# Kernel tuning notes

Measured on AMD Instinct MI355X. Metric: run time of the kernel, lower is better.

Reference implementation:

```python
import jax, jax.numpy as jnp
import numpy as np

B, NE, NN, L = 64, 256, 1024, 512
F_IN, HID = 128, 128
VOCAB = 50000
ALPHA = 0.2
NEG = -9.0e15


def _leaky(z):
    return jnp.where(z >= 0, z, ALPHA * z)


def hga_layer(x, adj, W, W2, W3, a, a2, wc, transfer, concat):
    # x: [B, NN, Fin], adj: [B, NE, NN] (hyperedge incidence)
    O = W2.shape[1]
    x4 = x @ W2                      # [B, NN, O]
    if transfer:
        x = x @ W                    # [B, NN, O]
    # node->edge attention: score depends only on node k (query is shared word_context)
    s0 = wc[0] @ a[:O, 0]            # scalar
    e1 = _leaky(x4 @ a[O:, 0] + s0)  # [B, NN]
    e1 = jnp.broadcast_to(e1[:, None, :], adj.shape)          # [B, NE, NN]
    att_edge = jax.nn.softmax(jnp.where(adj > 0, e1, NEG), axis=2)
    edge = att_edge @ x              # [B, NE, O]
    edge4 = edge @ W3                # [B, NE, O]
    # edge->node attention: query = node feat x4[k], key = edge feat edge4[j]
    e2 = _leaky((x4 @ a2[:O, 0])[:, None, :] + (edge4 @ a2[O:, 0])[:, :, None])  # [B, NE, NN]
    att_node = jax.nn.softmax(jnp.where(adj > 0, e2, NEG).transpose(0, 2, 1), axis=2)  # [B, NN, NE]
    node = att_node @ edge           # [B, NN, O]
    return jax.nn.elu(node) if concat else node


def setup_inputs() -> dict:
    key = jax.random.key(0)
    ks = jax.random.split(key, 16)
    stdv = 1.0 / np.sqrt(HID)
    u = lambda k, shape: jax.random.uniform(k, shape, jnp.float32, -stdv, stdv)
    inp = {
        "items": jax.random.randint(ks[0], (B, NN), 0, VOCAB),
        "alias_inputs": jax.random.randint(ks[1], (B, L), 0, NN),
        "node_masks": jnp.ones((B, L), jnp.float32),
        "adj": jax.random.randint(ks[2], (B, NE, NN), 0, 2).astype(jnp.float32),
        "emb": jax.random.normal(ks[3], (VOCAB, F_IN), jnp.float32),
        # layer 1 (transfer=False, concat=True)
        "w2_1": u(ks[4], (F_IN, HID)),
        "w3_1": u(ks[5], (HID, HID)),
        "a_1": u(ks[6], (2 * HID, 1)),
        "a2_1": u(ks[7], (2 * HID, 1)),
        "wc_1": u(ks[8], (1, HID)),
        # layer 2 (transfer=True, concat=False)
        "w_2": u(ks[9], (HID, HID)),
        "w2_2": u(ks[10], (HID, HID)),
        "w3_2": u(ks[11], (HID, HID)),
        "a_2": u(ks[12], (2 * HID, 1)),
        "a2_2": u(ks[13], (2 * HID, 1)),
        "wc_2": u(ks[14], (1, HID)),
        "ln_g": jnp.ones((HID,), jnp.float32),
        "ln_b": jnp.zeros((HID,), jnp.float32),
    }
    return inp


def reference(items, alias_inputs, node_masks, adj, emb,
              w2_1, w3_1, a_1, a2_1, wc_1,
              w_2, w2_2, w3_2, a_2, a2_2, wc_2,
              ln_g, ln_b):
    hidden = emb[items]                                        # [B, NN, F]
    x = hga_layer(hidden, adj, None, w2_1, w3_1, a_1, a2_1, wc_1,
                  transfer=False, concat=True)
    x = hga_layer(x, adj, w_2, w2_2, w3_2, a_2, a2_2, wc_2,
                  transfer=True, concat=False)                 # [B, NN, HID]
    seq = jnp.take_along_axis(x, alias_inputs[:, :, None], axis=1)  # [B, L, HID]
    m = node_masks[:, :, None]
    h = seq * m
    b = jnp.sum(h * m, axis=-2) / jnp.sum(node_masks, -1, keepdims=True)  # [B, HID]
    mu = jnp.mean(b, -1, keepdims=True)
    var = jnp.mean((b - mu) ** 2, -1, keepdims=True)
    return (b - mu) / jnp.sqrt(var + 1e-6) * ln_g + ln_b
```

## Files before the change

kernel.cpp:

```cpp
#include <hip/hip_runtime.h>
#include <hip/hip_bf16.h>

typedef __hip_bfloat16 bf16;
typedef __attribute__((ext_vector_type(8))) unsigned short u16x8;
typedef __attribute__((ext_vector_type(4))) unsigned short u16x4;
typedef __attribute__((ext_vector_type(4))) float f32x4;
typedef __attribute__((ext_vector_type(8))) short bf16x8;

#define B_   64
#define NE_  256
#define NN_  1024
#define L_   512
#define HID_ 128
#define ALPHA_ 0.2f

__device__ __forceinline__ float bfu(unsigned short u){
  unsigned int x = ((unsigned int)u) << 16;
  union { unsigned int i; float f; } c; c.i = x; return c.f;
}
__device__ __forceinline__ unsigned short f2b(float f){
  bf16 h = __float2bfloat16(f);
  union { bf16 b; unsigned short u; } c; c.b = h; return c.u;
}
__device__ __forceinline__ int swz(int r, int c){ return (c ^ (r & 3) ^ ((r >> 2) & 3)) & 3; }

__global__ void k_consts(const float* w2_1, const float* w3_1,
                         const float* a_1, const float* a2_1, const float* wc_1,
                         const float* w2_2, const float* w3_2,
                         const float* a_2, const float* a2_2, const float* wc_2,
                         const float* w_2,
                         float* consts, unsigned short* W2T)
{
  int blk = blockIdx.x, t = threadIdx.x;
  __shared__ float red[128];
  if (blk < 6) {
    const float* M; const float* v;
    switch (blk) {
      case 0: M = w2_1; v = a_1  + 128; break;
      case 1: M = w2_1; v = a2_1;       break;
      case 2: M = w3_1; v = a2_1 + 128; break;
      case 3: M = w2_2; v = a_2  + 128; break;
      case 4: M = w2_2; v = a2_2;       break;
      default: M = w3_2; v = a2_2 + 128; break;
    }
    float acc = 0.f;
    for (int o = 0; o < 128; ++o) acc += M[t*128 + o] * v[o];
    consts[blk*128 + t] = acc;
  } else if (blk < 8) {
    const float* wc = (blk == 6) ? wc_1 : wc_2;
    const float* a  = (blk == 6) ? a_1  : a_2;
    red[t] = wc[t] * a[t];
    __syncthreads();
    for (int s = 64; s > 0; s >>= 1) { if (t < s) red[t] += red[t + s]; __syncthreads(); }
    if (t == 0) consts[768 + (blk - 6)] = red[0];
  } else {
    for (int k = 0; k < 128; ++k) W2T[t*128 + k] = f2b(w_2[k*128 + t]);
  }
}

__global__ void k_prep(const float* __restrict__ adj,
                       unsigned long long* __restrict__ ADJBb,
                       unsigned long long* __restrict__ ADJTb)
{
  __shared__ unsigned char tile[64][68];
  __shared__ unsigned short pa[64][4];
  __shared__ unsigned short pt[64][4];
  int b  = blockIdx.z;
  int e0 = blockIdx.y * 64;
  int n0 = blockIdx.x * 64;
  int t  = threadIdx.x;
  int lr = t >> 2, lc0 = (t & 3) * 16;
  const float* src = adj + ((long)b*NE_ + e0 + lr)*NN_ + n0 + lc0;
  unsigned int mA = 0;
  #pragma unroll
  for (int j = 0; j < 16; j += 4) {
    f32x4 v = *(const f32x4*)(src + j);
    #pragma unroll
    for (int k = 0; k < 4; ++k) {
      unsigned char u = (v[k] != 0.f) ? 1 : 0;
      tile[lr][lc0+j+k] = u;
      mA |= ((unsigned int)u) << (j+k);
    }
  }
  pa[lr][t & 3] = (unsigned short)mA;
  __syncthreads();
  unsigned int mT = 0;
  #pragma unroll
  for (int j = 0; j < 16; ++j) mT |= ((unsigned int)tile[lc0 + j][lr]) << j;
  pt[lr][t & 3] = (unsigned short)mT;
  __syncthreads();
  if (t < 64) {
    unsigned long long wA = (unsigned long long)pa[t][0]
                          | ((unsigned long long)pa[t][1] << 16)
                          | ((unsigned long long)pa[t][2] << 32)
                          | ((unsigned long long)pa[t][3] << 48);
    ADJBb[((long)b*NE_ + e0 + t)*(NN_/64) + (n0 >> 6)] = wA;
    unsigned long long wT = (unsigned long long)pt[t][0]
                          | ((unsigned long long)pt[t][1] << 16)
                          | ((unsigned long long)pt[t][2] << 32)
                          | ((unsigned long long)pt[t][3] << 48);
    ADJTb[((long)b*NN_ + n0 + t)*(NE_/64) + (e0 >> 6)] = wT;
  }
}

__global__ void k_fproj(const float* __restrict__ emb, const int* __restrict__ gitems,
                        const float* __restrict__ consts,
                        float* __restrict__ w1, float* __restrict__ f1,
                        unsigned short* __restrict__ YT)
{
  __shared__ float ce1s[128], cf1s[128];
  __shared__ __attribute__((aligned(16))) unsigned short T[64][132];
  int b = blockIdx.y, n0 = blockIdx.x * 64, t = threadIdx.x;
  if (t < 128) { ce1s[t] = consts[t]; cf1s[t] = consts[128 + t]; }
  __syncthreads();
  int r = t >> 2, h0 = (t & 3) * 32;
  long row = (long)b*NN_ + n0 + r;
  float s0 = consts[768];
  float xv[32];
  const float* sp = emb + (long)gitems[row]*HID_ + h0;
  #pragma unroll
  for (int j = 0; j < 32; j += 4) {
    f32x4 v = *(const f32x4*)(sp + j);
    #pragma unroll
    for (int k = 0; k < 4; ++k) xv[j+k] = v[k];
  }
  float p1 = 0.f, p2 = 0.f;
  #pragma unroll
  for (int j = 0; j < 32; ++j) { p1 += xv[j]*ce1s[h0+j]; p2 += xv[j]*cf1s[h0+j]; }
  p1 += __shfl_xor(p1, 1, 4); p1 += __shfl_xor(p1, 2, 4);
  p2 += __shfl_xor(p2, 1, 4); p2 += __shfl_xor(p2, 2, 4);
  float z = p1 + s0; z = (z >= 0.f) ? z : ALPHA_*z;
  float w = __expf(z);
  if ((t & 3) == 0) { w1[row] = w; f1[row] = p2; }
  #pragma unroll
  for (int j = 0; j < 32; j += 4) {
    u16x4 o;
    #pragma unroll
    for (int k = 0; k < 4; ++k) o[k] = f2b(w * xv[j+k]);
    *(u16x4*)&T[r][h0+j] = o;
  }
  __syncthreads();
  int h = t >> 1, nh = (t & 1) * 32;
  unsigned short* dst = YT + ((long)b*HID_ + h)*NN_ + n0 + nh;
  #pragma unroll
  for (int j = 0; j < 32; j += 8) {
    u16x8 o;
    #pragma unroll
    for (int k = 0; k < 8; ++k) o[k] = T[nh+j+k][h];
    *(u16x8*)&dst[j] = o;
  }
}

template<int TRANSFER>
__global__ __launch_bounds__(256) void k_gemm_edge(
    const unsigned char* __restrict__ ADJ8,
    const unsigned short* __restrict__ YT,
    const float* __restrict__ w1v,
    const float* __restrict__ consts, int layer,
    const unsigned short* __restrict__ W2T,
    unsigned short* __restrict__ ET,
    float* __restrict__ f2o)
{
  __shared__ __attribute__((aligned(16))) unsigned short SM[12288];
  __shared__ float dsum[64];
  const int id = blockIdx.x;
  const int b = id & 63;
  const long e0 = (long)(id >> 6) * 64;
  const int t = threadIdx.x;
  const int lane = t & 63;
  const int w = t >> 6, wm = w >> 1, wn = w & 1;
  const int r4 = t >> 2, c4 = t & 3;
  const int lr = lane & 15, g = lane >> 4;

  f32x4 acc[2][4];
  #pragma unroll
  for (int i = 0; i < 2; ++i)
    #pragma unroll
    for (int j = 0; j < 4; ++j) acc[i][j] = (f32x4){0.f,0.f,0.f,0.f};

  const unsigned char*  Ab = ADJ8 + ((long)b*NE_ + e0 + r4)*(NN_ >> 3);
  const unsigned short* Bb = YT + (long)b*HID_*NN_;
  const float*          wb = w1v + (long)b*NN_;

  unsigned int ab; u16x8 bv0, bv1; f32x4 wv0, wv1;
  float dot = 0.f;

  auto stage = [&](int kc) {
    ab  = Ab[(kc >> 3) + c4];
    wv0 = *(const f32x4*)(wb + kc + c4*8);
    wv1 = *(const f32x4*)(wb + kc + c4*8 + 4);
    bv0 = *(const u16x8*)(Bb + (long)r4*NN_ + kc + c4*8);
    bv1 = *(const u16x8*)(Bb + (long)(64+r4)*NN_ + kc + c4*8);
  };
  auto commit = [&](int buf) {
    u16x8 av;
    #pragma unroll
    for (int j = 0; j < 8; ++j) {
      unsigned int bit = (ab >> j) & 1u;
      av[j] = bit ? (unsigned short)0x3F80 : (unsigned short)0;
      float wj = (j < 4) ? wv0[j] : wv1[j-4];
      dot += bit ? wj : 0.f;
    }
    *(u16x8*)&SM[buf*2048 + r4*32 + swz(r4,c4)*8] = av;
    *(u16x8*)&SM[4096 + buf*4096 + r4*32 + swz(r4,c4)*8] = bv0;
    *(u16x8*)&SM[4096 + buf*4096 + (64+r4)*32 + swz(64+r4,c4)*8] = bv1;
  };

  stage(0); commit(0);
  int cur = 0;
  const int NIT = NN_/32;
  for (int it = 0; it < NIT; ++it) {
    __syncthreads();
    if (it+1 < NIT) stage((it+1)*32);
    const unsigned short* AsB = &SM[cur*2048];
    const unsigned short* BsB = &SM[4096 + cur*4096];
    bf16x8 af[2], bfr[4];
    #pragma unroll
    for (int mt = 0; mt < 2; ++mt) {
      int r = wm*32 + mt*16 + lr;
      af[mt] = *(const bf16x8*)&AsB[r*32 + swz(r,g)*8];
    }
    #pragma unroll
    for (int nt = 0; nt < 4; ++nt) {
      int n = wn*64 + nt*16 + lr;
      bfr[nt] = *(const bf16x8*)&BsB[n*32 + swz(n,g)*8];
    }
    #pragma unroll
    for (int mt = 0; mt < 2; ++mt)
      #pragma unroll
      for (int nt = 0; nt < 4; ++nt)
        acc[mt][nt] = __builtin_amdgcn_mfma_f32_16x16x32_bf16(af[mt], bfr[nt], acc[mt][nt], 0, 0, 0);
    if (it+1 < NIT) { commit(cur^1); cur ^= 1; }
  }
  dot += __shfl_down(dot, 2, 4); dot += __shfl_down(dot, 1, 4);
  if ((lane & 3) == 0) dsum[r4] = dot;
  __syncthreads();
  #pragma unroll
  for (int mt = 0; mt < 2; ++mt)
    #pragma unroll
    for (int nt = 0; nt < 4; ++nt) {
      int col = wn*64 + nt*16 + lr;
      #pragma unroll
      for (int q = 0; q < 4; ++q) {
        int rl = wm*32 + mt*16 + g*4 + q;
        SM[rl*136 + col] = f2b(acc[mt][nt][q] / dsum[rl]);
      }
    }
  __syncthreads();
  if (TRANSFER) {
    f32x4 acc2[2][4];
    #pragma unroll
    for (int i = 0; i < 2; ++i)
      #pragma unroll
      for (int j = 0; j < 4; ++j) acc2[i][j] = (f32x4){0.f,0.f,0.f,0.f};
    #pragma unroll
    for (int kc2 = 0; kc2 < 4; ++kc2) {
      bf16x8 af[2], bfr[4];
      #pragma unroll
      for (int mt = 0; mt < 2; ++mt) {
        int r = wm*32 + mt*16 + lr;
        af[mt] = *(const bf16x8*)&SM[r*136 + kc2*32 + g*8];
      }
      #pragma unroll
      for (int nt = 0; nt < 4; ++nt) {
        int n = wn*64 + nt*16 + lr;
        bfr[nt] = *(const bf16x8*)(W2T + n*128 + kc2*32 + g*8);
      }
      #pragma unroll
      for (int mt = 0; mt < 2; ++mt)
        #pragma unroll
        for (int nt = 0; nt < 4; ++nt)
          acc2[mt][nt] = __builtin_amdgcn_mfma_f32_16x16x32_bf16(af[mt], bfr[nt], acc2[mt][nt], 0, 0, 0);
    }
    __syncthreads();
    #pragma unroll
    for (int mt = 0; mt < 2; ++mt)
      #pragma unroll
      for (int nt = 0; nt < 4; ++nt) {
        int col = wn*64 + nt*16 + lr;
        #pragma unroll
        for (int q = 0; q < 4; ++q) {
          int rl = wm*32 + mt*16 + g*4 + q;
          SM[rl*136 + col] = f2b(acc2[mt][nt][q]);
        }
      }
    __syncthreads();
  }
  {
    const float* cf2 = consts + layer*384 + 256;
    int r = t >> 2, h0 = (t & 3) * 32;
    float p = 0.f;
    #pragma unroll
    for (int j = 0; j < 32; ++j) p += bfu(SM[r*136 + h0 + j]) * cf2[h0 + j];
    p += __shfl_down(p, 2, 4); p += __shfl_down(p, 1, 4);
    if ((t & 3) == 0) f2o[(long)b*NE_ + e0 + r] = p;
  }
  {
    int h = t >> 1, eh = (t & 1) * 32;
    unsigned short* dst = ET + ((long)b*HID_ + h)*NE_ + e0 + eh;
    #pragma unroll
    for (int j = 0; j < 32; j += 8) {
      u16x8 o;
      #pragma unroll
      for (int k = 0; k < 8; ++k) o[k] = SM[(eh+j+k)*136 + h];
      *(u16x8*)&dst[j] = o;
    }
  }
}

template<int EPI>
__global__ __launch_bounds__(256, 2) void k_gemm_att(
    const unsigned char* __restrict__ ADJ8,
    const unsigned short* __restrict__ ET,
    const float* __restrict__ f1v, const float* __restrict__ f2v,
    const float* __restrict__ consts,
    unsigned short* __restrict__ YTout, float* __restrict__ w1o, float* __restrict__ f1o,
    const float* __restrict__ wcount, float* __restrict__ pooled)
{
  __shared__ __attribute__((aligned(16))) unsigned short SM[12288];
  __shared__ float dsum[64];
  __shared__ float colsum[128];
  __shared__ float wrow[64];
  const int id = blockIdx.x;
  const int b = id & 63;
  const long m0 = (long)(id >> 6) * 64;
  const int t = threadIdx.x;
  const int lane = t & 63;
  const int w = t >> 6, wm = w >> 1, wn = w & 1;
  const int r4 = t >> 2, c4 = t & 3;
  const int lr = lane & 15, g = lane >> 4;

  f32x4 acc[2][4];
  #pragma unroll
  for (int i = 0; i < 2; ++i)
    #pragma unroll
    for (int j = 0; j < 4; ++j) acc[i][j] = (f32x4){0.f,0.f,0.f,0.f};

  const float f1r = f1v[(long)b*NN_ + m0 + r4];
  const unsigned char*  Ab = ADJ8 + ((long)b*NN_ + m0 + r4)*(NE_ >> 3);
  const unsigned short* Bb = ET + (long)b*HID_*NE_;
  const float* f2p = f2v + (long)b*NE_;

  unsigned int ab; u16x8 bv0, bv1; f32x4 fv0, fv1;
  float dot = 0.f;

  auto stage = [&](int kc) {
    ab  = Ab[(kc >> 3) + c4];
    fv0 = *(const f32x4*)(f2p + kc + c4*8);
    fv1 = *(const f32x4*)(f2p + kc + c4*8 + 4);
    bv0 = *(const u16x8*)(Bb + (long)r4*NE_ + kc + c4*8);
    bv1 = *(const u16x8*)(Bb + (long)(64+r4)*NE_ + kc + c4*8);
  };
  auto commit = [&](int buf) {
    u16x8 av;
    #pragma unroll
    for (int j = 0; j < 8; ++j) {
      unsigned int bit = (ab >> j) & 1u;
      float z = f1r + ((j < 4) ? fv0[j] : fv1[j-4]);
      z = (z >= 0.f) ? z : ALPHA_ * z;
      float wt = bit ? __expf(z) : 0.f;
      unsigned short us = f2b(wt);
      av[j] = us; dot += bfu(us);
    }
    *(u16x8*)&SM[buf*2048 + r4*32 + swz(r4,c4)*8] = av;
    *(u16x8*)&SM[4096 + buf*4096 + r4*32 + swz(r4,c4)*8] = bv0;
    *(u16x8*)&SM[4096 + buf*4096 + (64+r4)*32 + swz(64+r4,c4)*8] = bv1;
  };

  stage(0); commit(0);
  int cur = 0;
  const int NIT = NE_/32;
  for (int it = 0; it < NIT; ++it) {
    __syncthreads();
    if (it+1 < NIT) stage((it+1)*32);
    const unsigned short* AsB = &SM[cur*2048];
    const unsigned short* BsB = &SM[4096 + cur*4096];
    bf16x8 af[2], bfr[4];
    #pragma unroll
    for (int mt = 0; mt < 2; ++mt) {
      int r = wm*32 + mt*16 + lr;
      af[mt] = *(const bf16x8*)&AsB[r*32 + swz(r,g)*8];
    }
    #pragma unroll
    for (int nt = 0; nt < 4; ++nt) {
      int n = wn*64 + nt*16 + lr;
      bfr[nt] = *(const bf16x8*)&BsB[n*32 + swz(n,g)*8];
    }
    #pragma unroll
    for (int mt = 0; mt < 2; ++mt)
      #pragma unroll
      for (int nt = 0; nt < 4; ++nt)
        acc[mt][nt] = __builtin_amdgcn_mfma_f32_16x16x32_bf16(af[mt], bfr[nt], acc[mt][nt], 0, 0, 0);
    if (it+1 < NIT) { commit(cur^1); cur ^= 1; }
  }
  dot += __shfl_down(dot, 2, 4); dot += __shfl_down(dot, 1, 4);
  if ((lane & 3) == 0) dsum[r4] = dot;
  if (EPI == 2 && t < 128) colsum[t] = 0.f;
  __syncthreads();

  if (EPI == 1) {
    #pragma unroll
    for (int mt = 0; mt < 2; ++mt)
      #pragma unroll
      for (int nt = 0; nt < 4; ++nt) {
        int col = wn*64 + nt*16 + lr;
        #pragma unroll
        for (int q = 0; q < 4; ++q) {
          int rl = wm*32 + mt*16 + g*4 + q;
          float v = acc[mt][nt][q] / dsum[rl];
          v = (v > 0.f) ? v : expm1f(v);
          SM[rl*136 + col] = f2b(v);
        }
      }
    __syncthreads();
    {
      const float* ce1 = consts + 384;
      const float* cf1 = consts + 512;
      int r = t >> 2, h0 = (t & 3) * 32;
      float p1 = 0.f, p2 = 0.f;
      #pragma unroll
      for (int j = 0; j < 32; ++j) {
        float xv = bfu(SM[r*136 + h0 + j]);
        p1 += xv * ce1[h0 + j];
        p2 += xv * cf1[h0 + j];
      }
      p1 += __shfl_down(p1, 2, 4); p1 += __shfl_down(p1, 1, 4);
      p2 += __shfl_down(p2, 2, 4); p2 += __shfl_down(p2, 1, 4);
      if ((t & 3) == 0) {
        float z = p1 + consts[769];
        z = (z >= 0.f) ? z : ALPHA_ * z;
        float wv = __expf(z);
        wrow[r] = wv;
        w1o[(long)b*NN_ + m0 + r] = wv;
        f1o[(long)b*NN_ + m0 + r] = p2;
      }
    }
    __syncthreads();
    {
      int h = t >> 1, nh = (t & 1) * 32;
      unsigned short* dst = YTout + ((long)b*HID_ + h)*NN_ + m0 + nh;
      #pragma unroll
      for (int j = 0; j < 32; j += 8) {
        u16x8 o;
        #pragma unroll
        for (int k = 0; k < 8; ++k) {
          int rr = nh + j + k;
          o[k] = f2b(wrow[rr] * bfu(SM[rr*136 + h]));
        }
        *(u16x8*)&dst[j] = o;
      }
    }
  } else {
    float psum[4] = {0.f, 0.f, 0.f, 0.f};
    #pragma unroll
    for (int mt = 0; mt < 2; ++mt)
      #pragma unroll
      for (int q = 0; q < 4; ++q) {
        int rl = wm*32 + mt*16 + g*4 + q;
        float wc = wcount[(long)b*NN_ + m0 + rl];
        float inv = wc / dsum[rl];
        #pragma unroll
        for (int nt = 0; nt < 4; ++nt) psum[nt] += inv * acc[mt][nt][q];
      }
    #pragma unroll
    for (int nt = 0; nt < 4; ++nt) atomicAdd(&colsum[wn*64 + nt*16 + lr], psum[nt]);
    __syncthreads();
    if (t < 128) atomicAdd(&pooled[(long)b*HID_ + t], colsum[t]);
  }
}

__global__ void k_zero(float* __restrict__ p, int n)
{
  int i = blockIdx.x*256 + threadIdx.x;
  if (i < n) p[i] = 0.f;
}

__global__ void k_wcount(const int* __restrict__ alias, const float* __restrict__ masks,
                         float* __restrict__ wcount, float* __restrict__ msum)
{
  int b = blockIdx.x, t = threadIdx.x;
  float m = masks[b*L_ + t];
  int idx = alias[b*L_ + t];
  atomicAdd(&wcount[(long)b*NN_ + idx], m*m);
  float s = m;
  #pragma unroll
  for (int sh = 32; sh > 0; sh >>= 1) s += __shfl_down(s, sh);
  __shared__ float red[8];
  if ((t & 63) == 0) red[t >> 6] = s;
  __syncthreads();
  if (t == 0) { float tot = 0.f; for (int i = 0; i < 8; ++i) tot += red[i]; msum[b] = tot; }
}

__global__ void k_ln(const float* __restrict__ pooled, const float* __restrict__ msum,
                     const float* __restrict__ ln_g, const float* __restrict__ ln_b,
                     float* __restrict__ out)
{
  int b = blockIdx.x, t = threadIdx.x;
  __shared__ float sr[2];
  float bv = pooled[b*HID_ + t] / msum[b];
  int lane = t & 63;
  float p = bv;
  #pragma unroll
  for (int s = 32; s > 0; s >>= 1) p += __shfl_xor(p, s);
  if (lane == 0) sr[t >> 6] = p;
  __syncthreads();
  float mu = (sr[0] + sr[1]) * (1.f / HID_);
  float dv = bv - mu;
  p = dv * dv;
  #pragma unroll
  for (int s = 32; s > 0; s >>= 1) p += __shfl_xor(p, s);
  __syncthreads();
  if (lane == 0) sr[t >> 6] = p;
  __syncthreads();
  float var = (sr[0] + sr[1]) * (1.f / HID_);
  out[b*HID_ + t] = dv / sqrtf(var + 1e-6f) * ln_g[t] + ln_b[t];
}

extern "C" void kernel_launch(void* const* d_in, const int* in_sizes, int n_in,
                              void* d_out, int out_size, void* d_ws, size_t ws_size,
                              hipStream_t stream)
{
  const int*   items = (const int*)d_in[0];
  const int*   alias = (const int*)d_in[1];
  const float* masks = (const float*)d_in[2];
  const float* adj   = (const float*)d_in[3];
  const float* emb   = (const float*)d_in[4];
  const float* w2_1  = (const float*)d_in[5];
  const float* w3_1  = (const float*)d_in[6];
  const float* a_1   = (const float*)d_in[7];
  const float* a2_1  = (const float*)d_in[8];
  const float* wc_1  = (const float*)d_in[9];
  const float* w_2   = (const float*)d_in[10];
  const float* w2_2  = (const float*)d_in[11];
  const float* w3_2  = (const float*)d_in[12];
  const float* a_2   = (const float*)d_in[13];
  const float* a2_2  = (const float*)d_in[14];
  const float* wc_2  = (const float*)d_in[15];
  const float* ln_g  = (const float*)d_in[16];
  const float* ln_b  = (const float*)d_in[17];
  float* out = (float*)d_out;

  char* ws = (char*)d_ws;
  size_t off = 0;
  auto alloc = [&](size_t bytes) -> void* {
    void* p = ws + off; off += (bytes + 255) / 256 * 256; return p;
  };
  unsigned long long* ADJBb = (unsigned long long*)alloc((size_t)B_*NE_*(NN_/8));
  unsigned long long* ADJTb = (unsigned long long*)alloc((size_t)B_*NN_*(NE_/8));
  unsigned short* YT   = (unsigned short*)alloc((size_t)B_*HID_*NN_*2);
  unsigned short* ET   = (unsigned short*)alloc((size_t)B_*HID_*NE_*2);
  float* wcount= (float*)alloc((size_t)B_*NN_*4);
  float* pooled= (float*)alloc((size_t)B_*HID_*4);
  float* w1L1  = (float*)alloc((size_t)B_*NN_*4);
  float* f1L1  = (float*)alloc((size_t)B_*NN_*4);
  float* w1L2  = (float*)alloc((size_t)B_*NN_*4);
  float* f1L2  = (float*)alloc((size_t)B_*NN_*4);
  float* f2    = (float*)alloc((size_t)B_*NE_*4);
  float* msum  = (float*)alloc(B_*4);
  float* consts= (float*)alloc(772*4);
  unsigned short* W2T = (unsigned short*)alloc((size_t)HID_*HID_*2);
  if (off > ws_size) return;

  const int kZeroN = B_*NN_ + B_*HID_;

  k_consts<<<9, 128, 0, stream>>>(w2_1, w3_1, a_1, a2_1, wc_1, w2_2, w3_2, a_2, a2_2, wc_2,
                                  w_2, consts, W2T);
  k_zero<<<(kZeroN + 255)/256, 256, 0, stream>>>(wcount, kZeroN);
  k_wcount<<<B_, L_, 0, stream>>>(alias, masks, wcount, msum);
  k_prep<<<dim3(NN_/64, NE_/64, B_), 256, 0, stream>>>(adj, ADJBb, ADJTb);

  k_fproj<<<dim3(NN_/64, B_), 256, 0, stream>>>(emb, items, consts, w1L1, f1L1, YT);
  k_gemm_edge<0><<<B_*(NE_/64), 256, 0, stream>>>((const unsigned char*)ADJBb, YT, w1L1,
        consts, 0, W2T, ET, f2);
  k_gemm_att<1><<<B_*(NN_/64), 256, 0, stream>>>((const unsigned char*)ADJTb, ET, f1L1, f2,
        consts, YT, w1L2, f1L2, nullptr, nullptr);

  k_gemm_edge<1><<<B_*(NE_/64), 256, 0, stream>>>((const unsigned char*)ADJBb, YT, w1L2,
        consts, 1, W2T, ET, f2);
  k_gemm_att<2><<<B_*(NN_/64), 256, 0, stream>>>((const unsigned char*)ADJTb, ET, f1L2, f2,
        consts, nullptr, nullptr, nullptr, wcount, pooled);

  k_ln<<<B_, HID_, 0, stream>>>(pooled, msum, ln_g, ln_b, out);
}
```

Before: 133.6 us.

## Merge front-end prep kernels into one launch with block-range dispatch

```diff
diff --git a/kernel.cpp b/kernel.cpp
--- a/kernel.cpp
+++ b/kernel.cpp
@@ -24,130 +24,184 @@
 }
 __device__ __forceinline__ int swz(int r, int c){ return (c ^ (r & 3) ^ ((r >> 2) & 3)) & 3; }
 
-__global__ void k_consts(const float* w2_1, const float* w3_1,
-                         const float* a_1, const float* a2_1, const float* wc_1,
-                         const float* w2_2, const float* w3_2,
-                         const float* a_2, const float* a2_2, const float* wc_2,
-                         const float* w_2,
-                         float* consts, unsigned short* W2T)
+__global__ __launch_bounds__(256) void k_front(
+    const float* __restrict__ adj,
+    unsigned long long* __restrict__ ADJBb, unsigned long long* __restrict__ ADJTb,
+    const float* __restrict__ emb, const int* __restrict__ items,
+    const float* __restrict__ w2_1, const float* __restrict__ w3_1,
+    const float* __restrict__ a_1,  const float* __restrict__ a2_1,
+    const float* __restrict__ wc_1,
+    const float* __restrict__ w_2,
+    const float* __restrict__ w2_2, const float* __restrict__ w3_2,
+    const float* __restrict__ a_2,  const float* __restrict__ a2_2,
+    const float* __restrict__ wc_2,
+    const int* __restrict__ alias, const float* __restrict__ masks,
+    float* __restrict__ w1L1, float* __restrict__ f1L1,
+    unsigned short* __restrict__ YT,
+    float* __restrict__ consts, unsigned short* __restrict__ W2T,
+    float* __restrict__ wcount, float* __restrict__ msum, float* __restrict__ pooled)
 {
-  int blk = blockIdx.x, t = threadIdx.x;
-  __shared__ float red[128];
-  if (blk < 6) {
-    const float* M; const float* v;
-    switch (blk) {
-      case 0: M = w2_1; v = a_1  + 128; break;
-      case 1: M = w2_1; v = a2_1;       break;
-      case 2: M = w3_1; v = a2_1 + 128; break;
-      case 3: M = w2_2; v = a_2  + 128; break;
-      case 4: M = w2_2; v = a2_2;       break;
-      default: M = w3_2; v = a2_2 + 128; break;
-    }
-    float acc = 0.f;
-    for (int o = 0; o < 128; ++o) acc += M[t*128 + o] * v[o];
-    consts[blk*128 + t] = acc;
-  } else if (blk < 8) {
-    const float* wc = (blk == 6) ? wc_1 : wc_2;
-    const float* a  = (blk == 6) ? a_1  : a_2;
-    red[t] = wc[t] * a[t];
-    __syncthreads();
-    for (int s = 64; s > 0; s >>= 1) { if (t < s) red[t] += red[t + s]; __syncthreads(); }
-    if (t == 0) consts[768 + (blk - 6)] = red[0];
+  __shared__ __attribute__((aligned(16))) unsigned char SMEM[18432];
+  const int id = blockIdx.x;
+  const int t  = threadIdx.x;
+
+  if (id < 4096) {
+    unsigned char (*tile)[68] = (unsigned char(*)[68])SMEM;
+    unsigned short (*pa)[4] = (unsigned short(*)[4])(SMEM + 4608);
+    unsigned short (*pt)[4] = (unsigned short(*)[4])(SMEM + 5120);
+    int b  = id >> 6;
+    int e0 = ((id >> 4) & 3) * 64;
+    int n0 = (id & 15) * 64;
+    int lr = t >> 2, lc0 = (t & 3) * 16;
+    const float* src = adj + ((long)b*NE_ + e0 + lr)*NN_ + n0 + lc0;
+    unsigned int mA = 0;
+    #pragma unroll
+    for (int j = 0; j < 16; j += 4) {
+      f32x4 v = *(const f32x4*)(src + j);
+      #pragma unroll
+      for (int k = 0; k < 4; ++k) {
+        unsigned char u = (v[k] != 0.f) ? 1 : 0;
+        tile[lr][lc0+j+k] = u;
+        mA |= ((unsigned int)u) << (j+k);
+      }
+    }
+    pa[lr][t & 3] = (unsigned short)mA;
+    __syncthreads();
+    unsigned int mT = 0;
+    #pragma unroll
+    for (int j = 0; j < 16; ++j) mT |= ((unsigned int)tile[lc0 + j][lr]) << j;
+    pt[lr][t & 3] = (unsigned short)mT;
+    __syncthreads();
+    if (t < 64) {
+      unsigned long long wA = (unsigned long long)pa[t][0]
+                            | ((unsigned long long)pa[t][1] << 16)
+                            | ((unsigned long long)pa[t][2] << 32)
+                            | ((unsigned long long)pa[t][3] << 48);
+      ADJBb[((long)b*NE_ + e0 + t)*(NN_/64) + (n0 >> 6)] = wA;
+      unsigned long long wT = (unsigned long long)pt[t][0]
+                            | ((unsigned long long)pt[t][1] << 16)
+                            | ((unsigned long long)pt[t][2] << 32)
+                            | ((unsigned long long)pt[t][3] << 48);
+      ADJTb[((long)b*NN_ + n0 + t)*(NE_/64) + (e0 >> 6)] = wT;
+    }
+  } else if (id < 5120) {
+    float* ce1s = (float*)SMEM;
+    float* cf1s = (float*)(SMEM + 512);
+    float* s0s  = (float*)(SMEM + 1024);
+    unsigned short (*T)[132] = (unsigned short(*)[132])(SMEM + 1040 + 8);
+    T = (unsigned short(*)[132])(SMEM + 1056);
+    {
+      int rr = t & 127;
+      const float* Mrow = w2_1 + rr*128;
+      const float* vv = (t < 128) ? (a_1 + 128) : a2_1;
+      float acc = 0.f;
+      #pragma unroll 4
+      for (int o = 0; o < 128; o += 4) {
+        f32x4 m = *(const f32x4*)(Mrow + o);
+        f32x4 x = *(const f32x4*)(vv + o);
+        acc += m[0]*x[0] + m[1]*x[1] + m[2]*x[2] + m[3]*x[3];
+      }
+      if (t < 128) ce1s[rr] = acc; else cf1s[rr] = acc;
+      if (t < 64) {
+        float s = wc_1[t]*a_1[t] + wc_1[t+64]*a_1[t+64];
+        #pragma unroll
+        for (int sh = 32; sh > 0; sh >>= 1) s += __shfl_xor(s, sh);
+        if (t == 0) s0s[0] = s;
+      }
+    }
+    __syncthreads();
+    int fid = id - 4096;
+    int b = fid >> 4, n0 = (fid & 15) * 64;
+    int r = t >> 2, h0 = (t & 3) * 32;
+    long row = (long)b*NN_ + n0 + r;
+    float s0 = s0s[0];
+    float xv[32];
+    const float* sp = emb + (long)items[row]*HID_ + h0;
+    #pragma unroll
+    for (int j = 0; j < 32; j += 4) {
+      f32x4 v = *(const f32x4*)(sp + j);
+      #pragma unroll
+      for (int k = 0; k < 4; ++k) xv[j+k] = v[k];
+    }
+    float p1 = 0.f, p2 = 0.f;
+    #pragma unroll
+    for (int j = 0; j < 32; ++j) { p1 += xv[j]*ce1s[h0+j]; p2 += xv[j]*cf1s[h0+j]; }
+    p1 += __shfl_xor(p1, 1, 4); p1 += __shfl_xor(p1, 2, 4);
+    p2 += __shfl_xor(p2, 1, 4); p2 += __shfl_xor(p2, 2, 4);
+    float z = p1 + s0; z = (z >= 0.f) ? z : ALPHA_*z;
+    float w = __expf(z);
+    if ((t & 3) == 0) { w1L1[row] = w; f1L1[row] = p2; }
+    #pragma unroll
+    for (int j = 0; j < 32; j += 4) {
+      u16x4 o;
+      #pragma unroll
+      for (int k = 0; k < 4; ++k) o[k] = f2b(w * xv[j+k]);
+      *(u16x4*)&T[r][h0+j] = o;
+    }
+    __syncthreads();
+    int h = t >> 1, nh = (t & 1) * 32;
+    unsigned short* dst = YT + ((long)b*HID_ + h)*NN_ + n0 + nh;
+    #pragma unroll
+    for (int j = 0; j < 32; j += 8) {
+      u16x8 o;
+      #pragma unroll
+      for (int k = 0; k < 8; ++k) o[k] = T[nh+j+k][h];
+      *(u16x8*)&dst[j] = o;
+    }
+  } else if (id < 5129) {
+    float* red = (float*)SMEM;
+    int blk = id - 5120;
+    if (t >= 128) { __syncthreads(); return; }
+    if (blk < 6) {
+      const float* M; const float* v;
+      switch (blk) {
+        case 0: M = w2_1; v = a_1  + 128; break;
+        case 1: M = w2_1; v = a2_1;       break;
+        case 2: M = w3_1; v = a2_1 + 128; break;
+        case 3: M = w2_2; v = a_2  + 128; break;
+        case 4: M = w2_2; v = a2_2;       break;
+        default: M = w3_2; v = a2_2 + 128; break;
+      }
+      float acc = 0.f;
+      for (int o = 0; o < 128; ++o) acc += M[t*128 + o] * v[o];
+      consts[blk*128 + t] = acc;
+      __syncthreads();
+    } else if (blk < 8) {
+      const float* wc = (blk == 6) ? wc_1 : wc_2;
+      const float* a  = (blk == 6) ? a_1  : a_2;
+      red[t] = wc[t] * a[t];
+      __syncthreads();
+      for (int s = 64; s > 0; s >>= 1) { if (t < s) red[t] += red[t + s]; __syncthreads(); }
+      if (t == 0) consts[768 + (blk - 6)] = red[0];
+    } else {
+      for (int k = 0; k < 128; ++k) W2T[t*128 + k] = f2b(w_2[k*128 + t]);
+      __syncthreads();
+    }
+  } else if (id < 5193) {
+    float* wc = (float*)SMEM;
+    float* red = (float*)(SMEM + 4096);
+    int b = id - 5129;
+    #pragma unroll
+    for (int j = 0; j < 4; ++j) wc[t + j*256] = 0.f;
+    __syncthreads();
+    float s = 0.f;
+    #pragma unroll
+    for (int j = 0; j < 2; ++j) {
+      int l = t + j*256;
+      float m = masks[b*L_ + l];
+      int idx = alias[b*L_ + l];
+      atomicAdd(&wc[idx], m*m);
+      s += m;
+    }
+    #pragma unroll
+    for (int sh = 32; sh > 0; sh >>= 1) s += __shfl_xor(s, sh);
+    if ((t & 63) == 0) red[t >> 6] = s;
+    __syncthreads();
+    if (t == 0) msum[b] = red[0] + red[1] + red[2] + red[3];
+    #pragma unroll
+    for (int j = 0; j < 4; ++j) wcount[(long)b*NN_ + t + j*256] = wc[t + j*256];
   } else {
-    for (int k = 0; k < 128; ++k) W2T[t*128 + k] = f2b(w_2[k*128 + t]);
-  }
-}
-
-__global__ void k_prep(const float* __restrict__ adj,
-                       unsigned long long* __restrict__ ADJBb,
-                       unsigned long long* __restrict__ ADJTb)
-{
-  __shared__ unsigned char tile[64][68];
-  __shared__ unsigned short pa[64][4];
-  __shared__ unsigned short pt[64][4];
-  int b  = blockIdx.z;
-  int e0 = blockIdx.y * 64;
-  int n0 = blockIdx.x * 64;
-  int t  = threadIdx.x;
-  int lr = t >> 2, lc0 = (t & 3) * 16;
-  const float* src = adj + ((long)b*NE_ + e0 + lr)*NN_ + n0 + lc0;
-  unsigned int mA = 0;
-  #pragma unroll
-  for (int j = 0; j < 16; j += 4) {
-    f32x4 v = *(const f32x4*)(src + j);
-    #pragma unroll
-    for (int k = 0; k < 4; ++k) {
-      unsigned char u = (v[k] != 0.f) ? 1 : 0;
-      tile[lr][lc0+j+k] = u;
-      mA |= ((unsigned int)u) << (j+k);
-    }
-  }
-  pa[lr][t & 3] = (unsigned short)mA;
-  __syncthreads();
-  unsigned int mT = 0;
-  #pragma unroll
-  for (int j = 0; j < 16; ++j) mT |= ((unsigned int)tile[lc0 + j][lr]) << j;
-  pt[lr][t & 3] = (unsigned short)mT;
-  __syncthreads();
-  if (t < 64) {
-    unsigned long long wA = (unsigned long long)pa[t][0]
-                          | ((unsigned long long)pa[t][1] << 16)
-                          | ((unsigned long long)pa[t][2] << 32)
-                          | ((unsigned long long)pa[t][3] << 48);
-    ADJBb[((long)b*NE_ + e0 + t)*(NN_/64) + (n0 >> 6)] = wA;
-    unsigned long long wT = (unsigned long long)pt[t][0]
-                          | ((unsigned long long)pt[t][1] << 16)
-                          | ((unsigned long long)pt[t][2] << 32)
-                          | ((unsigned long long)pt[t][3] << 48);
-    ADJTb[((long)b*NN_ + n0 + t)*(NE_/64) + (e0 >> 6)] = wT;
-  }
-}
-
-__global__ void k_fproj(const float* __restrict__ emb, const int* __restrict__ gitems,
-                        const float* __restrict__ consts,
-                        float* __restrict__ w1, float* __restrict__ f1,
-                        unsigned short* __restrict__ YT)
-{
-  __shared__ float ce1s[128], cf1s[128];
-  __shared__ __attribute__((aligned(16))) unsigned short T[64][132];
-  int b = blockIdx.y, n0 = blockIdx.x * 64, t = threadIdx.x;
-  if (t < 128) { ce1s[t] = consts[t]; cf1s[t] = consts[128 + t]; }
-  __syncthreads();
-  int r = t >> 2, h0 = (t & 3) * 32;
-  long row = (long)b*NN_ + n0 + r;
-  float s0 = consts[768];
-  float xv[32];
-  const float* sp = emb + (long)gitems[row]*HID_ + h0;
-  #pragma unroll
-  for (int j = 0; j < 32; j += 4) {
-    f32x4 v = *(const f32x4*)(sp + j);
-    #pragma unroll
-    for (int k = 0; k < 4; ++k) xv[j+k] = v[k];
-  }
-  float p1 = 0.f, p2 = 0.f;
-  #pragma unroll
-  for (int j = 0; j < 32; ++j) { p1 += xv[j]*ce1s[h0+j]; p2 += xv[j]*cf1s[h0+j]; }
-  p1 += __shfl_xor(p1, 1, 4); p1 += __shfl_xor(p1, 2, 4);
-  p2 += __shfl_xor(p2, 1, 4); p2 += __shfl_xor(p2, 2, 4);
-  float z = p1 + s0; z = (z >= 0.f) ? z : ALPHA_*z;
-  float w = __expf(z);
-  if ((t & 3) == 0) { w1[row] = w; f1[row] = p2; }
-  #pragma unroll
-  for (int j = 0; j < 32; j += 4) {
-    u16x4 o;
-    #pragma unroll
-    for (int k = 0; k < 4; ++k) o[k] = f2b(w * xv[j+k]);
-    *(u16x4*)&T[r][h0+j] = o;
-  }
-  __syncthreads();
-  int h = t >> 1, nh = (t & 1) * 32;
-  unsigned short* dst = YT + ((long)b*HID_ + h)*NN_ + n0 + nh;
-  #pragma unroll
-  for (int j = 0; j < 32; j += 8) {
-    u16x8 o;
-    #pragma unroll
-    for (int k = 0; k < 8; ++k) o[k] = T[nh+j+k][h];
-    *(u16x8*)&dst[j] = o;
+    for (int i = t; i < B_*HID_; i += 256) pooled[i] = 0.f;
   }
 }
 
@@ -467,28 +521,6 @@
     __syncthreads();
     if (t < 128) atomicAdd(&pooled[(long)b*HID_ + t], colsum[t]);
   }
-}
-
-__global__ void k_zero(float* __restrict__ p, int n)
-{
-  int i = blockIdx.x*256 + threadIdx.x;
-  if (i < n) p[i] = 0.f;
-}
-
-__global__ void k_wcount(const int* __restrict__ alias, const float* __restrict__ masks,
-                         float* __restrict__ wcount, float* __restrict__ msum)
-{
-  int b = blockIdx.x, t = threadIdx.x;
-  float m = masks[b*L_ + t];
-  int idx = alias[b*L_ + t];
-  atomicAdd(&wcount[(long)b*NN_ + idx], m*m);
-  float s = m;
-  #pragma unroll
-  for (int sh = 32; sh > 0; sh >>= 1) s += __shfl_down(s, sh);
-  __shared__ float red[8];
-  if ((t & 63) == 0) red[t >> 6] = s;
-  __syncthreads();
-  if (t == 0) { float tot = 0.f; for (int i = 0; i < 8; ++i) tot += red[i]; msum[b] = tot; }
 }
 
 __global__ void k_ln(const float* __restrict__ pooled, const float* __restrict__ msum,
@@ -561,15 +593,10 @@
   unsigned short* W2T = (unsigned short*)alloc((size_t)HID_*HID_*2);
   if (off > ws_size) return;
 
-  const int kZeroN = B_*NN_ + B_*HID_;
-
-  k_consts<<<9, 128, 0, stream>>>(w2_1, w3_1, a_1, a2_1, wc_1, w2_2, w3_2, a_2, a2_2, wc_2,
-                                  w_2, consts, W2T);
-  k_zero<<<(kZeroN + 255)/256, 256, 0, stream>>>(wcount, kZeroN);
-  k_wcount<<<B_, L_, 0, stream>>>(alias, masks, wcount, msum);
-  k_prep<<<dim3(NN_/64, NE_/64, B_), 256, 0, stream>>>(adj, ADJBb, ADJTb);
-
-  k_fproj<<<dim3(NN_/64, B_), 256, 0, stream>>>(emb, items, consts, w1L1, f1L1, YT);
+  k_front<<<5194, 256, 0, stream>>>(adj, ADJBb, ADJTb, emb, items,
+        w2_1, w3_1, a_1, a2_1, wc_1, w_2, w2_2, w3_2, a_2, a2_2, wc_2,
+        alias, masks, w1L1, f1L1, YT, consts, W2T, wcount, msum, pooled);
+
   k_gemm_edge<0><<<B_*(NE_/64), 256, 0, stream>>>((const unsigned char*)ADJBb, YT, w1L1,
         consts, 0, W2T, ET, f2);
   k_gemm_att<1><<<B_*(NN_/64), 256, 0, stream>>>((const unsigned char*)ADJTb, ET, f1L1, f2,
```

New measurement: 139.5 us. 4.4% more time.

## Merge setup kernels into one launch and rewrite adjacency bit-packing transpose

Applied to the files above, without the earlier changes.

```diff
diff --git a/kernel.cpp b/kernel.cpp
--- a/kernel.cpp
+++ b/kernel.cpp
@@ -24,82 +24,112 @@
 }
 __device__ __forceinline__ int swz(int r, int c){ return (c ^ (r & 3) ^ ((r >> 2) & 3)) & 3; }
 
-__global__ void k_consts(const float* w2_1, const float* w3_1,
-                         const float* a_1, const float* a2_1, const float* wc_1,
-                         const float* w2_2, const float* w3_2,
-                         const float* a_2, const float* a2_2, const float* wc_2,
-                         const float* w_2,
-                         float* consts, unsigned short* W2T)
-{
+__global__ void k_small(const float* __restrict__ w2_1, const float* __restrict__ w3_1,
+                        const float* __restrict__ a_1,  const float* __restrict__ a2_1,
+                        const float* __restrict__ wc_1,
+                        const float* __restrict__ w2_2, const float* __restrict__ w3_2,
+                        const float* __restrict__ a_2,  const float* __restrict__ a2_2,
+                        const float* __restrict__ wc_2,
+                        const float* __restrict__ w_2,
+                        const int* __restrict__ alias, const float* __restrict__ masks,
+                        float* __restrict__ consts, unsigned short* __restrict__ W2T,
+                        float* __restrict__ wcount, float* __restrict__ msum,
+                        float* __restrict__ pooled)
+{
+  __shared__ float wcs[1024];
+  __shared__ float red4[4];
   int blk = blockIdx.x, t = threadIdx.x;
-  __shared__ float red[128];
   if (blk < 6) {
-    const float* M; const float* v;
-    switch (blk) {
-      case 0: M = w2_1; v = a_1  + 128; break;
-      case 1: M = w2_1; v = a2_1;       break;
-      case 2: M = w3_1; v = a2_1 + 128; break;
-      case 3: M = w2_2; v = a_2  + 128; break;
-      case 4: M = w2_2; v = a2_2;       break;
-      default: M = w3_2; v = a2_2 + 128; break;
-    }
-    float acc = 0.f;
-    for (int o = 0; o < 128; ++o) acc += M[t*128 + o] * v[o];
-    consts[blk*128 + t] = acc;
+    if (t < 128) {
+      const float* M; const float* v;
+      switch (blk) {
+        case 0: M = w2_1; v = a_1  + 128; break;
+        case 1: M = w2_1; v = a2_1;       break;
+        case 2: M = w3_1; v = a2_1 + 128; break;
+        case 3: M = w2_2; v = a_2  + 128; break;
+        case 4: M = w2_2; v = a2_2;       break;
+        default: M = w3_2; v = a2_2 + 128; break;
+      }
+      float acc = 0.f;
+      #pragma unroll 4
+      for (int o = 0; o < 128; o += 4) {
+        f32x4 m = *(const f32x4*)(M + t*128 + o);
+        f32x4 x = *(const f32x4*)(v + o);
+        acc += m[0]*x[0] + m[1]*x[1] + m[2]*x[2] + m[3]*x[3];
+      }
+      consts[blk*128 + t] = acc;
+    }
   } else if (blk < 8) {
     const float* wc = (blk == 6) ? wc_1 : wc_2;
     const float* a  = (blk == 6) ? a_1  : a_2;
-    red[t] = wc[t] * a[t];
-    __syncthreads();
-    for (int s = 64; s > 0; s >>= 1) { if (t < s) red[t] += red[t + s]; __syncthreads(); }
-    if (t == 0) consts[768 + (blk - 6)] = red[0];
+    if (t < 64) {
+      float s = wc[t]*a[t] + wc[t+64]*a[t+64];
+      #pragma unroll
+      for (int sh = 32; sh > 0; sh >>= 1) s += __shfl_xor(s, sh);
+      if (t == 0) consts[768 + (blk - 6)] = s;
+    }
+  } else if (blk == 8) {
+    if (t < 128) for (int k = 0; k < 128; ++k) W2T[t*128 + k] = f2b(w_2[k*128 + t]);
+  } else if (blk == 9) {
+    for (int i = t; i < B_*HID_; i += 256) pooled[i] = 0.f;
   } else {
-    for (int k = 0; k < 128; ++k) W2T[t*128 + k] = f2b(w_2[k*128 + t]);
-  }
-}
-
-__global__ void k_prep(const float* __restrict__ adj,
-                       unsigned long long* __restrict__ ADJBb,
-                       unsigned long long* __restrict__ ADJTb)
-{
-  __shared__ unsigned char tile[64][68];
-  __shared__ unsigned short pa[64][4];
-  __shared__ unsigned short pt[64][4];
-  int b  = blockIdx.z;
-  int e0 = blockIdx.y * 64;
-  int n0 = blockIdx.x * 64;
-  int t  = threadIdx.x;
-  int lr = t >> 2, lc0 = (t & 3) * 16;
-  const float* src = adj + ((long)b*NE_ + e0 + lr)*NN_ + n0 + lc0;
-  unsigned int mA = 0;
-  #pragma unroll
-  for (int j = 0; j < 16; j += 4) {
+    int b = blk - 10;
+    #pragma unroll
+    for (int j = 0; j < 4; ++j) wcs[t + j*256] = 0.f;
+    __syncthreads();
+    float s = 0.f;
+    #pragma unroll
+    for (int j = 0; j < 2; ++j) {
+      int l = t + j*256;
+      float m = masks[b*L_ + l];
+      int idx = alias[b*L_ + l];
+      atomicAdd(&wcs[idx], m*m);
+      s += m;
+    }
+    #pragma unroll
+    for (int sh = 32; sh > 0; sh >>= 1) s += __shfl_xor(s, sh);
+    if ((t & 63) == 0) red4[t >> 6] = s;
+    __syncthreads();
+    if (t == 0) msum[b] = red4[0] + red4[1] + red4[2] + red4[3];
+    #pragma unroll
+    for (int j = 0; j < 4; ++j) wcount[(long)b*NN_ + t + j*256] = wcs[t + j*256];
+  }
+}
+
+__global__ __launch_bounds__(256) void k_prep(
+    const float* __restrict__ adj,
+    unsigned long long* __restrict__ ADJBb,
+    unsigned short* __restrict__ ADJT16)
+{
+  __shared__ unsigned long long Lbits[16][17];
+  const int id = blockIdx.x;
+  const int b  = id & 63;
+  const int ec = id >> 6;
+  const int t  = threadIdx.x;
+  const int r  = t >> 4;
+  const int c  = t & 15;
+  const int e  = ec*16 + r;
+  const float* src = adj + ((long)b*NE_ + e)*NN_ + c*64;
+  unsigned long long m = 0;
+  #pragma unroll
+  for (int j = 0; j < 64; j += 4) {
     f32x4 v = *(const f32x4*)(src + j);
     #pragma unroll
-    for (int k = 0; k < 4; ++k) {
-      unsigned char u = (v[k] != 0.f) ? 1 : 0;
-      tile[lr][lc0+j+k] = u;
-      mA |= ((unsigned int)u) << (j+k);
-    }
-  }
-  pa[lr][t & 3] = (unsigned short)mA;
-  __syncthreads();
-  unsigned int mT = 0;
-  #pragma unroll
-  for (int j = 0; j < 16; ++j) mT |= ((unsigned int)tile[lc0 + j][lr]) << j;
-  pt[lr][t & 3] = (unsigned short)mT;
-  __syncthreads();
-  if (t < 64) {
-    unsigned long long wA = (unsigned long long)pa[t][0]
-                          | ((unsigned long long)pa[t][1] << 16)
-                          | ((unsigned long long)pa[t][2] << 32)
-                          | ((unsigned long long)pa[t][3] << 48);
-    ADJBb[((long)b*NE_ + e0 + t)*(NN_/64) + (n0 >> 6)] = wA;
-    unsigned long long wT = (unsigned long long)pt[t][0]
-                          | ((unsigned long long)pt[t][1] << 16)
-                          | ((unsigned long long)pt[t][2] << 32)
-                          | ((unsigned long long)pt[t][3] << 48);
-    ADJTb[((long)b*NN_ + n0 + t)*(NE_/64) + (e0 >> 6)] = wT;
+    for (int k = 0; k < 4; ++k)
+      m |= (unsigned long long)(v[k] != 0.f) << (j + k);
+  }
+  ADJBb[((long)b*NE_ + e)*16 + c] = m;
+  Lbits[r][c] = m;
+  __syncthreads();
+  #pragma unroll
+  for (int j = 0; j < 4; ++j) {
+    int n = t + 256*j;
+    int w = n >> 6, bitn = n & 63;
+    unsigned int o = 0;
+    #pragma unroll
+    for (int rr = 0; rr < 16; ++rr)
+      o |= (unsigned int)((Lbits[rr][w] >> bitn) & 1ull) << rr;
+    ADJT16[((long)b*NN_ + n)*16 + ec] = (unsigned short)o;
   }
 }
 
@@ -467,28 +497,6 @@
     __syncthreads();
     if (t < 128) atomicAdd(&pooled[(long)b*HID_ + t], colsum[t]);
   }
-}
-
-__global__ void k_zero(float* __restrict__ p, int n)
-{
-  int i = blockIdx.x*256 + threadIdx.x;
-  if (i < n) p[i] = 0.f;
-}
-
-__global__ void k_wcount(const int* __restrict__ alias, const float* __restrict__ masks,
-                         float* __restrict__ wcount, float* __restrict__ msum)
-{
-  int b = blockIdx.x, t = threadIdx.x;
-  float m = masks[b*L_ + t];
-  int idx = alias[b*L_ + t];
-  atomicAdd(&wcount[(long)b*NN_ + idx], m*m);
-  float s = m;
-  #pragma unroll
-  for (int sh = 32; sh > 0; sh >>= 1) s += __shfl_down(s, sh);
-  __shared__ float red[8];
-  if ((t & 63) == 0) red[t >> 6] = s;
-  __syncthreads();
-  if (t == 0) { float tot = 0.f; for (int i = 0; i < 8; ++i) tot += red[i]; msum[b] = tot; }
 }
 
 __global__ void k_ln(const float* __restrict__ pooled, const float* __restrict__ msum,
@@ -546,7 +554,7 @@
     void* p = ws + off; off += (bytes + 255) / 256 * 256; return p;
   };
   unsigned long long* ADJBb = (unsigned long long*)alloc((size_t)B_*NE_*(NN_/8));
-  unsigned long long* ADJTb = (unsigned long long*)alloc((size_t)B_*NN_*(NE_/8));
+  unsigned short*     ADJT16= (unsigned short*)    alloc((size_t)B_*NN_*(NE_/8));
   unsigned short* YT   = (unsigned short*)alloc((size_t)B_*HID_*NN_*2);
   unsigned short* ET   = (unsigned short*)alloc((size_t)B_*HID_*NE_*2);
   float* wcount= (float*)alloc((size_t)B_*NN_*4);
@@ -561,23 +569,19 @@
   unsigned short* W2T = (unsigned short*)alloc((size_t)HID_*HID_*2);
   if (off > ws_size) return;
 
-  const int kZeroN = B_*NN_ + B_*HID_;
-
-  k_consts<<<9, 128, 0, stream>>>(w2_1, w3_1, a_1, a2_1, wc_1, w2_2, w3_2, a_2, a2_2, wc_2,
-                                  w_2, consts, W2T);
-  k_zero<<<(kZeroN + 255)/256, 256, 0, stream>>>(wcount, kZeroN);
-  k_wcount<<<B_, L_, 0, stream>>>(alias, masks, wcount, msum);
-  k_prep<<<dim3(NN_/64, NE_/64, B_), 256, 0, stream>>>(adj, ADJBb, ADJTb);
-
+  k_small<<<74, 256, 0, stream>>>(w2_1, w3_1, a_1, a2_1, wc_1, w2_2, w3_2, a_2, a2_2, wc_2,
+                                  w_2, alias, masks, consts, W2T, wcount, msum, pooled);
+  k_prep<<<B_*16, 256, 0, stream>>>(adj, ADJBb, ADJT16);
   k_fproj<<<dim3(NN_/64, B_), 256, 0, stream>>>(emb, items, consts, w1L1, f1L1, YT);
+
   k_gemm_edge<0><<<B_*(NE_/64), 256, 0, stream>>>((const unsigned char*)ADJBb, YT, w1L1,
         consts, 0, W2T, ET, f2);
-  k_gemm_att<1><<<B_*(NN_/64), 256, 0, stream>>>((const unsigned char*)ADJTb, ET, f1L1, f2,
+  k_gemm_att<1><<<B_*(NN_/64), 256, 0, stream>>>((const unsigned char*)ADJT16, ET, f1L1, f2,
         consts, YT, w1L2, f1L2, nullptr, nullptr);
 
   k_gemm_edge<1><<<B_*(NE_/64), 256, 0, stream>>>((const unsigned char*)ADJBb, YT, w1L2,
         consts, 1, W2T, ET, f2);
-  k_gemm_att<2><<<B_*(NN_/64), 256, 0, stream>>>((const unsigned char*)ADJTb, ET, f1L2, f2,
+  k_gemm_att<2><<<B_*(NN_/64), 256, 0, stream>>>((const unsigned char*)ADJT16, ET, f1L2, f2,
         consts, nullptr, nullptr, nullptr, wcount, pooled);
 
   k_ln<<<B_, HID_, 0, stream>>>(pooled, msum, ln_g, ln_b, out);
```

After: 130.2 us. 2.6% less time.
